# Kernel optimization log

Hardware: AMD Instinct MI355X
Metric: run time of the kernel (lower is better)

The kernel has to match this reference:

```python
import jax, jax.numpy as jnp
import numpy as np

FEATURE_DIM, HIDDEN_DIM, ATTN_DIM = 2048, 1024, 1024
B, L = 128, 196


def setup_inputs() -> dict:
    key = jax.random.key(0)
    ks = jax.random.split(key, 8)
    s_enc = 1.0 / np.sqrt(FEATURE_DIM)
    s_hid = 1.0 / np.sqrt(HIDDEN_DIM)
    s_full = 1.0 / np.sqrt(ATTN_DIM)
    return {
        "encoder_out": jax.random.normal(ks[0], (B, L, FEATURE_DIM), jnp.float32),
        "hidden": jax.random.normal(ks[1], (B, HIDDEN_DIM), jnp.float32),
        "W_enc": jax.random.uniform(ks[2], (FEATURE_DIM, ATTN_DIM), jnp.float32, -s_enc, s_enc),
        "b_enc": jax.random.uniform(ks[3], (ATTN_DIM,), jnp.float32, -s_enc, s_enc),
        "W_hid": jax.random.uniform(ks[4], (HIDDEN_DIM, ATTN_DIM), jnp.float32, -s_hid, s_hid),
        "b_hid": jax.random.uniform(ks[5], (ATTN_DIM,), jnp.float32, -s_hid, s_hid),
        "W_full": jax.random.uniform(ks[6], (ATTN_DIM,), jnp.float32, -s_full, s_full),
        "b_full": jax.random.uniform(ks[7], (1,), jnp.float32, -s_full, s_full),
    }


def reference(encoder_out, hidden, W_enc, b_enc, W_hid, b_hid, W_full, b_full):
    # attn1: (B, L, A)
    attn1 = jnp.einsum("blf,fa->bla", encoder_out, W_enc) + b_enc
    # attn2: (B, 1, A)
    attn2 = (hidden @ W_hid + b_hid)[:, None, :]
    attn = jax.nn.relu(attn1 + attn2)
    # scalar score per location: (B, L)
    scores = jnp.einsum("bla,a->bl", attn, W_full) + b_full[0]
    alpha = jax.nn.softmax(scores, axis=1)
    # weighted sum over L: (B, F)
    context = jnp.einsum("blf,bl->bf", encoder_out, alpha)
    return context, alpha
```

## Files before the change

kernel.cpp:

```cpp
#include <hip/hip_runtime.h>
#include <hip/hip_bf16.h>

typedef unsigned short u16;
typedef short s16x8 __attribute__((ext_vector_type(8)));
typedef unsigned int u32x4 __attribute__((ext_vector_type(4)));
typedef float f32x4 __attribute__((ext_vector_type(4)));

#define F_DIM 2048
#define A_DIM 1024
#define H_DIM 1024
#define BATCH 128
#define LLEN  196
#define MROWS (BATCH * LLEN)

__device__ __forceinline__ u16 f2b(float x) {
  union { float f; unsigned int u; } c; c.f = x;
  unsigned int r = (c.u + 0x7fffu + ((c.u >> 16) & 1u)) >> 16;
  return (u16)r;
}

__device__ __forceinline__ unsigned int f2b_pk(float a, float b) {
  unsigned int r;
  asm volatile("v_cvt_pk_bf16_f32 %0, %1, %2" : "=v"(r) : "v"(a), "v"(b));
  return r;
}

__device__ __forceinline__ void gload_lds16(const void* g, void* l) {
  __builtin_amdgcn_global_load_lds((const __attribute__((address_space(1))) void*)g,
                                   (__attribute__((address_space(3))) void*)l, 16, 0, 0);
}

__global__ void wenc_cvt_kernel(const float* __restrict__ W, u16* __restrict__ WT) {
  __shared__ float tile[32][33];
  int kb = blockIdx.x * 32, ab = blockIdx.y * 32;
  int t = threadIdx.x;
  int r = t >> 3, c = (t & 7) * 4;
  float4 v = *(const float4*)&W[(size_t)(kb + r) * A_DIM + ab + c];
  tile[r][c] = v.x; tile[r][c + 1] = v.y; tile[r][c + 2] = v.z; tile[r][c + 3] = v.w;
  __syncthreads();
  ushort4 o;
  o.x = f2b(tile[c + 0][r]);
  o.y = f2b(tile[c + 1][r]);
  o.z = f2b(tile[c + 2][r]);
  o.w = f2b(tile[c + 3][r]);
  *(ushort4*)&WT[(size_t)(ab + r) * F_DIM + kb + c] = o;
}

__global__ void attn2_kernel(const float* __restrict__ hidden, const float* __restrict__ W_hid,
                             const float* __restrict__ b_hid, const float* __restrict__ b_enc,
                             float* __restrict__ attn2p) {
  __shared__ float hl[8][128];
  int t = threadIdx.x;
  int a  = blockIdx.x * 256 + t;
  int b0 = blockIdx.y * 8;
  int k0 = blockIdx.z * 128;
  {
    int j = t >> 5, kk = (t & 31) * 4;
    float4 v = *(const float4*)&hidden[(size_t)(b0 + j) * H_DIM + k0 + kk];
    hl[j][kk + 0] = v.x; hl[j][kk + 1] = v.y; hl[j][kk + 2] = v.z; hl[j][kk + 3] = v.w;
  }
  __syncthreads();
  float acc[8] = {0.f, 0.f, 0.f, 0.f, 0.f, 0.f, 0.f, 0.f};
  #pragma unroll 4
  for (int k = 0; k < 128; ++k) {
    float w = W_hid[(size_t)(k0 + k) * A_DIM + a];
    #pragma unroll
    for (int j = 0; j < 8; ++j) acc[j] = fmaf(hl[j][k], w, acc[j]);
  }
  if (blockIdx.z == 0) {
    float bias = b_hid[a] + b_enc[a];
    #pragma unroll
    for (int j = 0; j < 8; ++j) acc[j] += bias;
  }
  #pragma unroll
  for (int j = 0; j < 8; ++j) atomicAdd(&attn2p[(size_t)(b0 + j) * A_DIM + a], acc[j]);
}

__global__ void gemm_score(const float* __restrict__ enc, const u16* __restrict__ WT,
                           const float* __restrict__ attn2p, const float* __restrict__ W_full,
                           float* __restrict__ scores) {
  __shared__ __align__(16) float Asf[128 * 32];
  __shared__ __align__(16) u16 Bs[128 * 32];
  __shared__ float wf_lds[128];
  __shared__ float at2_lds[2][128];

  int i = blockIdx.x;
  int g  = i >> 6;
  int r  = i & 63;
  int y  = r >> 3;
  int gi = r & 7;
  int mt = g * 8 + gi;
  if (mt >= MROWS / 128) return;

  int n0 = y * 128;
  int m0 = mt * 128;
  int t = threadIdx.x;

  int b0 = m0 / LLEN;
  int bnd = (b0 + 1) * LLEN;
  int b1 = min(b0 + 1, BATCH - 1);

  if (t < 128) {
    wf_lds[t] = W_full[n0 + t];
    at2_lds[0][t] = attn2p[(size_t)b0 * A_DIM + n0 + t];
    at2_lds[1][t] = attn2p[(size_t)b1 * A_DIM + n0 + t];
  }

  int lane = t & 63, wave = t >> 6;
  int wr = wave >> 1, wc = wave & 1;
  int c16 = lane & 15, quad = lane >> 4;

  f32x4 acc[4][4];
  #pragma unroll
  for (int ii = 0; ii < 4; ++ii)
    #pragma unroll
    for (int j = 0; j < 4; ++j) acc[ii][j] = (f32x4){0.f, 0.f, 0.f, 0.f};

  const float* agp = enc + (size_t)(m0 + wave * 32 + (lane >> 3)) * F_DIM
                         + ((lane & 7) ^ ((lane >> 3) & 7)) * 4;
  float* al = Asf + wave * 1024;
  const u16* bgp = WT + (size_t)(n0 + (t >> 2)) * F_DIM + ((t & 3) ^ ((t >> 3) & 3)) * 8;
  u16* bl = Bs + wave * 512;

  int akey = c16 & 7;
  int bkey = (c16 >> 1) & 3;

  for (int kt = 0; kt < F_DIM; kt += 32) {
    gload_lds16(agp + kt, al);
    gload_lds16(agp + (size_t)8 * F_DIM + kt, al + 256);
    gload_lds16(agp + (size_t)16 * F_DIM + kt, al + 512);
    gload_lds16(agp + (size_t)24 * F_DIM + kt, al + 768);
    gload_lds16(bgp + kt, bl);
    gload_lds16(bgp + (size_t)64 * F_DIM + kt, bl + 2048);
    __syncthreads();
    s16x8 af[4], bf[4];
    #pragma unroll
    for (int ii = 0; ii < 4; ++ii) {
      int arow = (wr * 64 + ii * 16 + c16) * 32;
      float4 lo = *(const float4*)&Asf[arow + ((2 * quad) ^ akey) * 4];
      float4 hi = *(const float4*)&Asf[arow + ((2 * quad + 1) ^ akey) * 4];
      u32x4 w;
      w.x = f2b_pk(lo.x, lo.y);
      w.y = f2b_pk(lo.z, lo.w);
      w.z = f2b_pk(hi.x, hi.y);
      w.w = f2b_pk(hi.z, hi.w);
      af[ii] = __builtin_bit_cast(s16x8, w);
      bf[ii] = *(const s16x8*)&Bs[(wc * 64 + ii * 16 + c16) * 32 + (quad ^ bkey) * 8];
    }
    #pragma unroll
    for (int mi = 0; mi < 4; ++mi)
      #pragma unroll
      for (int ni = 0; ni < 4; ++ni)
        acc[mi][ni] = __builtin_amdgcn_mfma_f32_16x16x32_bf16(af[mi], bf[ni], acc[mi][ni], 0, 0, 0);
    __syncthreads();
  }

  float wf[4], a2a[4], a2b[4];
  #pragma unroll
  for (int ni = 0; ni < 4; ++ni) {
    int col = wc * 64 + ni * 16 + c16;
    wf[ni] = wf_lds[col];
    a2a[ni] = at2_lds[0][col];
    a2b[ni] = at2_lds[1][col];
  }
  #pragma unroll
  for (int mi = 0; mi < 4; ++mi) {
    #pragma unroll
    for (int rr = 0; rr < 4; ++rr) {
      int row_g = m0 + wr * 64 + mi * 16 + quad * 4 + rr;
      bool hi = row_g >= bnd;
      float p = 0.f;
      #pragma unroll
      for (int ni = 0; ni < 4; ++ni) {
        float v = acc[mi][ni][rr] + (hi ? a2b[ni] : a2a[ni]);
        v = fmaxf(v, 0.f);
        p = fmaf(v, wf[ni], p);
      }
      p += __shfl_xor(p, 1);
      p += __shfl_xor(p, 2);
      p += __shfl_xor(p, 4);
      p += __shfl_xor(p, 8);
      if (c16 == 0) atomicAdd(&scores[row_g], p);
    }
  }
}

__global__ void softmax_kernel(const float* __restrict__ scores, float* __restrict__ alpha) {
  __shared__ float red[8];
  int b = blockIdx.x, t = threadIdx.x;
  float s = (t < LLEN) ? scores[b * LLEN + t] : -3.0e38f;
  float m = s;
  #pragma unroll
  for (int o = 1; o <= 32; o <<= 1) m = fmaxf(m, __shfl_xor(m, o));
  if ((t & 63) == 0) red[t >> 6] = m;
  __syncthreads();
  m = fmaxf(fmaxf(red[0], red[1]), fmaxf(red[2], red[3]));
  float e = (t < LLEN) ? expf(s - m) : 0.f;
  float sum = e;
  #pragma unroll
  for (int o = 1; o <= 32; o <<= 1) sum += __shfl_xor(sum, o);
  __syncthreads();
  if ((t & 63) == 0) red[4 + (t >> 6)] = sum;
  __syncthreads();
  sum = red[4] + red[5] + red[6] + red[7];
  if (t < LLEN) alpha[b * LLEN + t] = e / sum;
}

__global__ void context_kernel(const float* __restrict__ enc, const float* __restrict__ alpha,
                               float* __restrict__ out) {
  __shared__ float al[49];
  int b = blockIdx.y, t = threadIdx.x;
  int l0 = blockIdx.z * 49;
  int f4 = blockIdx.x * 256 + t;
  if (t < 49) al[t] = alpha[b * LLEN + l0 + t];
  __syncthreads();
  const float4* e4 = (const float4*)enc + ((size_t)b * LLEN + l0) * (F_DIM / 4) + f4;
  float4 acc = {0.f, 0.f, 0.f, 0.f};
  #pragma unroll 7
  for (int l = 0; l < 49; ++l) {
    float4 v = e4[(size_t)l * (F_DIM / 4)];
    float a = al[l];
    acc.x = fmaf(v.x, a, acc.x);
    acc.y = fmaf(v.y, a, acc.y);
    acc.z = fmaf(v.z, a, acc.z);
    acc.w = fmaf(v.w, a, acc.w);
  }
  float* o = out + (size_t)b * F_DIM + f4 * 4;
  atomicAdd(o + 0, acc.x);
  atomicAdd(o + 1, acc.y);
  atomicAdd(o + 2, acc.z);
  atomicAdd(o + 3, acc.w);
}

extern "C" void kernel_launch(void* const* d_in, const int* in_sizes, int n_in,
                              void* d_out, int out_size, void* d_ws, size_t ws_size,
                              hipStream_t stream) {
  const float* enc    = (const float*)d_in[0];
  const float* hidden = (const float*)d_in[1];
  const float* W_enc  = (const float*)d_in[2];
  const float* b_enc  = (const float*)d_in[3];
  const float* W_hid  = (const float*)d_in[4];
  const float* b_hid  = (const float*)d_in[5];
  const float* W_full = (const float*)d_in[6];
  float* out = (float*)d_out;
  float* alpha_out = out + (size_t)BATCH * F_DIM;

  const size_t wt_bytes = (size_t)A_DIM * F_DIM * sizeof(u16);
  const size_t a2_bytes = (size_t)BATCH * A_DIM * sizeof(float);
  const size_t sc_bytes = (size_t)MROWS * sizeof(float);
  char* ws = (char*)d_ws;
  u16*   WT     = (u16*)ws;
  float* attn2p = (float*)(ws + wt_bytes);
  float* scores = (float*)(ws + wt_bytes + a2_bytes);

  hipMemsetAsync(attn2p, 0, a2_bytes, stream);
  hipMemsetAsync(scores, 0, sc_bytes, stream);
  hipMemsetAsync(out, 0, (size_t)BATCH * F_DIM * sizeof(float), stream);

  wenc_cvt_kernel<<<dim3(F_DIM / 32, A_DIM / 32), 256, 0, stream>>>(W_enc, WT);
  attn2_kernel<<<dim3(A_DIM / 256, BATCH / 8, H_DIM / 128), 256, 0, stream>>>(hidden, W_hid, b_hid, b_enc, attn2p);
  gemm_score<<<dim3(1600), 256, 0, stream>>>(enc, WT, attn2p, W_full, scores);
  softmax_kernel<<<dim3(BATCH), 256, 0, stream>>>(scores, alpha_out);
  context_kernel<<<dim3(2, BATCH, 4), 256, 0, stream>>>(enc, alpha_out, out);
}
```

Before: 499.4 us.

## Rewrite score GEMM with 256x256 tiles and 4-stage register/LDS pipeline

The fused score GEMM now uses 256x256 output tiles with 512-thread blocks, which cuts redundant reloads of the fp32 encoder tile and of the bf16 weights. Encoder data is prefetched into registers, converted to bf16 once, and stored to LDS, so the per-wave repeated fp32-to-bf16 conversion at fragment load goes away. A 4-deep LDS ring with loads issued two to four k-steps ahead overlaps memory traffic with MFMA work, and s_setprio raises priority during the MFMA burst. The epilogue handles tiles that span up to three batch rows. In exchange, register pressure goes up with 32 accumulators per thread plus prefetch registers, LDS use grows to 128KB per block, and the grid shrinks to 416 blocks, which may hurt occupancy and load balance.

```diff
diff --git a/kernel.cpp b/kernel.cpp
--- a/kernel.cpp
+++ b/kernel.cpp
@@ -3,7 +3,7 @@
 
 typedef unsigned short u16;
 typedef short s16x8 __attribute__((ext_vector_type(8)));
-typedef unsigned int u32x4 __attribute__((ext_vector_type(4)));
+typedef unsigned int u32x2 __attribute__((ext_vector_type(2)));
 typedef float f32x4 __attribute__((ext_vector_type(4)));
 
 #define F_DIM 2048
@@ -12,6 +12,7 @@
 #define BATCH 128
 #define LLEN  196
 #define MROWS (BATCH * LLEN)
+#define MTILES (MROWS / 256)
 
 __device__ __forceinline__ u16 f2b(float x) {
   union { float f; unsigned int u; } c; c.f = x;
@@ -76,103 +77,137 @@
   for (int j = 0; j < 8; ++j) atomicAdd(&attn2p[(size_t)(b0 + j) * A_DIM + a], acc[j]);
 }
 
-__global__ void gemm_score(const float* __restrict__ enc, const u16* __restrict__ WT,
-                           const float* __restrict__ attn2p, const float* __restrict__ W_full,
-                           float* __restrict__ scores) {
-  __shared__ __align__(16) float Asf[128 * 32];
-  __shared__ __align__(16) u16 Bs[128 * 32];
-  __shared__ float wf_lds[128];
-  __shared__ float at2_lds[2][128];
+__global__ __launch_bounds__(512, 2) void gemm_score(
+    const float* __restrict__ enc, const u16* __restrict__ WT,
+    const float* __restrict__ attn2p, const float* __restrict__ W_full,
+    float* __restrict__ scores) {
+  __shared__ __align__(16) u16 As[4 * 8192];
+  __shared__ __align__(16) u16 Bs[4 * 8192];
 
   int i = blockIdx.x;
-  int g  = i >> 6;
-  int r  = i & 63;
-  int y  = r >> 3;
-  int gi = r & 7;
+  int g = i >> 5, r = i & 31;
+  int y = r >> 3, gi = r & 7;
   int mt = g * 8 + gi;
-  if (mt >= MROWS / 128) return;
-
-  int n0 = y * 128;
-  int m0 = mt * 128;
+  if (mt >= MTILES) return;
+  int m0 = mt * 256, n0 = y * 256;
   int t = threadIdx.x;
-
-  int b0 = m0 / LLEN;
-  int bnd = (b0 + 1) * LLEN;
-  int b1 = min(b0 + 1, BATCH - 1);
-
-  if (t < 128) {
-    wf_lds[t] = W_full[n0 + t];
-    at2_lds[0][t] = attn2p[(size_t)b0 * A_DIM + n0 + t];
-    at2_lds[1][t] = attn2p[(size_t)b1 * A_DIM + n0 + t];
-  }
-
   int lane = t & 63, wave = t >> 6;
-  int wr = wave >> 1, wc = wave & 1;
+  int wr = wave >> 2, wc = wave & 3;
   int c16 = lane & 15, quad = lane >> 4;
 
-  f32x4 acc[4][4];
-  #pragma unroll
-  for (int ii = 0; ii < 4; ++ii)
+  const float* aP = enc + (size_t)(m0 + (t >> 3)) * F_DIM + (t & 7) * 4;
+  const int awoff = (t >> 3) * 32 + ((((t & 7) >> 1) ^ (((t >> 3) >> 1) & 3)) * 8)
+                  + ((t & 7) & 1) * 4;
+  const u16* bP = WT + (size_t)(n0 + (t >> 2)) * F_DIM + ((t & 3) ^ ((t >> 3) & 3)) * 8;
+  const int bw512 = wave * 512;
+
+  const int akey = (c16 >> 1) & 3;
+  const int aroff = (wr * 128 + c16) * 32 + (quad ^ akey) * 8;
+  const int broff = (wc * 64 + c16) * 32 + (quad ^ akey) * 8;
+
+  f32x4 acc[8][4];
+  #pragma unroll
+  for (int mi = 0; mi < 8; ++mi)
     #pragma unroll
-    for (int j = 0; j < 4; ++j) acc[ii][j] = (f32x4){0.f, 0.f, 0.f, 0.f};
-
-  const float* agp = enc + (size_t)(m0 + wave * 32 + (lane >> 3)) * F_DIM
-                         + ((lane & 7) ^ ((lane >> 3) & 7)) * 4;
-  float* al = Asf + wave * 1024;
-  const u16* bgp = WT + (size_t)(n0 + (t >> 2)) * F_DIM + ((t & 3) ^ ((t >> 3) & 3)) * 8;
-  u16* bl = Bs + wave * 512;
-
-  int akey = c16 & 7;
-  int bkey = (c16 >> 1) & 3;
-
-  for (int kt = 0; kt < F_DIM; kt += 32) {
-    gload_lds16(agp + kt, al);
-    gload_lds16(agp + (size_t)8 * F_DIM + kt, al + 256);
-    gload_lds16(agp + (size_t)16 * F_DIM + kt, al + 512);
-    gload_lds16(agp + (size_t)24 * F_DIM + kt, al + 768);
-    gload_lds16(bgp + kt, bl);
-    gload_lds16(bgp + (size_t)64 * F_DIM + kt, bl + 2048);
-    __syncthreads();
-    s16x8 af[4], bf[4];
-    #pragma unroll
-    for (int ii = 0; ii < 4; ++ii) {
-      int arow = (wr * 64 + ii * 16 + c16) * 32;
-      float4 lo = *(const float4*)&Asf[arow + ((2 * quad) ^ akey) * 4];
-      float4 hi = *(const float4*)&Asf[arow + ((2 * quad + 1) ^ akey) * 4];
-      u32x4 w;
-      w.x = f2b_pk(lo.x, lo.y);
-      w.y = f2b_pk(lo.z, lo.w);
-      w.z = f2b_pk(hi.x, hi.y);
-      w.w = f2b_pk(hi.z, hi.w);
-      af[ii] = __builtin_bit_cast(s16x8, w);
-      bf[ii] = *(const s16x8*)&Bs[(wc * 64 + ii * 16 + c16) * 32 + (quad ^ bkey) * 8];
-    }
-    #pragma unroll
-    for (int mi = 0; mi < 4; ++mi)
-      #pragma unroll
-      for (int ni = 0; ni < 4; ++ni)
-        acc[mi][ni] = __builtin_amdgcn_mfma_f32_16x16x32_bf16(af[mi], bf[ni], acc[mi][ni], 0, 0, 0);
-    __syncthreads();
-  }
-
-  float wf[4], a2a[4], a2b[4];
+    for (int ni = 0; ni < 4; ++ni) acc[mi][ni] = (f32x4){0.f, 0.f, 0.f, 0.f};
+
+  float4 R0[4], R1[4];
+
+  #pragma unroll
+  for (int ii = 0; ii < 4; ++ii) R0[ii] = *(const float4*)(aP + (size_t)ii * 64 * F_DIM);
+  #pragma unroll
+  for (int ii = 0; ii < 4; ++ii) R1[ii] = *(const float4*)(aP + (size_t)ii * 64 * F_DIM + 32);
+  gload_lds16(bP, &Bs[bw512]);
+  gload_lds16(bP + (size_t)128 * F_DIM, &Bs[4096 + bw512]);
+  gload_lds16(bP + 32, &Bs[8192 + bw512]);
+  gload_lds16(bP + (size_t)128 * F_DIM + 32, &Bs[8192 + 4096 + bw512]);
+  #pragma unroll
+  for (int ii = 0; ii < 4; ++ii) {
+    u32x2 w; w.x = f2b_pk(R0[ii].x, R0[ii].y); w.y = f2b_pk(R0[ii].z, R0[ii].w);
+    *(u32x2*)&As[awoff + ii * 2048] = w;
+  }
+  #pragma unroll
+  for (int ii = 0; ii < 4; ++ii) {
+    u32x2 w; w.x = f2b_pk(R1[ii].x, R1[ii].y); w.y = f2b_pk(R1[ii].z, R1[ii].w);
+    *(u32x2*)&As[8192 + awoff + ii * 2048] = w;
+  }
+  #pragma unroll
+  for (int ii = 0; ii < 4; ++ii) R0[ii] = *(const float4*)(aP + (size_t)ii * 64 * F_DIM + 64);
+  #pragma unroll
+  for (int ii = 0; ii < 4; ++ii) R1[ii] = *(const float4*)(aP + (size_t)ii * 64 * F_DIM + 96);
+  asm volatile("s_waitcnt vmcnt(0) lgkmcnt(0)" ::: "memory");
+  __builtin_amdgcn_s_barrier();
+
+#define TILE(J, RX) do {                                                        \
+    const int rb_ = (J) * 8192;                                                 \
+    const int wb_ = (((J) + 2) & 3) * 8192;                                     \
+    int p_ = kt + (J);                                                          \
+    int kts_ = min(p_ + 2, 63);                                                 \
+    int ktl_ = min(p_ + 4, 63);                                                 \
+    _Pragma("unroll")                                                           \
+    for (int ii = 0; ii < 4; ++ii) {                                            \
+      u32x2 w_; w_.x = f2b_pk(RX[ii].x, RX[ii].y);                              \
+      w_.y = f2b_pk(RX[ii].z, RX[ii].w);                                        \
+      *(u32x2*)&As[wb_ + awoff + ii * 2048] = w_;                               \
+    }                                                                           \
+    _Pragma("unroll")                                                           \
+    for (int ii = 0; ii < 4; ++ii)                                              \
+      RX[ii] = *(const float4*)(aP + (size_t)ii * 64 * F_DIM + ktl_ * 32);      \
+    gload_lds16(bP + (size_t)kts_ * 32, &Bs[wb_ + bw512]);                      \
+    gload_lds16(bP + (size_t)128 * F_DIM + (size_t)kts_ * 32,                   \
+                &Bs[wb_ + 4096 + bw512]);                                       \
+    {                                                                           \
+      s16x8 af_[8], bf_[4];                                                     \
+      _Pragma("unroll")                                                         \
+      for (int ni = 0; ni < 4; ++ni)                                            \
+        bf_[ni] = *(const s16x8*)&Bs[rb_ + broff + ni * 512];                   \
+      _Pragma("unroll")                                                         \
+      for (int mi = 0; mi < 8; ++mi)                                            \
+        af_[mi] = *(const s16x8*)&As[rb_ + aroff + mi * 512];                   \
+      __builtin_amdgcn_s_setprio(1);                                            \
+      _Pragma("unroll")                                                         \
+      for (int mi = 0; mi < 8; ++mi)                                            \
+        _Pragma("unroll")                                                       \
+        for (int ni = 0; ni < 4; ++ni)                                          \
+          acc[mi][ni] = __builtin_amdgcn_mfma_f32_16x16x32_bf16(                \
+              af_[mi], bf_[ni], acc[mi][ni], 0, 0, 0);                          \
+      __builtin_amdgcn_s_setprio(0);                                            \
+    }                                                                           \
+    asm volatile("s_waitcnt vmcnt(6) lgkmcnt(0)" ::: "memory");                 \
+    __builtin_amdgcn_s_barrier();                                               \
+  } while (0)
+
+  #pragma unroll 1
+  for (int kt = 0; kt < 64; kt += 4) {
+    TILE(0, R0);
+    TILE(1, R1);
+    TILE(2, R0);
+    TILE(3, R1);
+  }
+#undef TILE
+
+  int bfirst = m0 / LLEN;
+  int bnd1 = (bfirst + 1) * LLEN, bnd2 = (bfirst + 2) * LLEN;
+  int b1c = min(bfirst + 1, BATCH - 1), b2c = min(bfirst + 2, BATCH - 1);
+  float wf[4], a2v0[4], a2v1[4], a2v2[4];
   #pragma unroll
   for (int ni = 0; ni < 4; ++ni) {
-    int col = wc * 64 + ni * 16 + c16;
-    wf[ni] = wf_lds[col];
-    a2a[ni] = at2_lds[0][col];
-    a2b[ni] = at2_lds[1][col];
-  }
-  #pragma unroll
-  for (int mi = 0; mi < 4; ++mi) {
+    int col = n0 + wc * 64 + ni * 16 + c16;
+    wf[ni]   = W_full[col];
+    a2v0[ni] = attn2p[(size_t)bfirst * A_DIM + col];
+    a2v1[ni] = attn2p[(size_t)b1c * A_DIM + col];
+    a2v2[ni] = attn2p[(size_t)b2c * A_DIM + col];
+  }
+  #pragma unroll
+  for (int mi = 0; mi < 8; ++mi) {
     #pragma unroll
     for (int rr = 0; rr < 4; ++rr) {
-      int row_g = m0 + wr * 64 + mi * 16 + quad * 4 + rr;
-      bool hi = row_g >= bnd;
+      int row_g = m0 + wr * 128 + mi * 16 + quad * 4 + rr;
       float p = 0.f;
       #pragma unroll
       for (int ni = 0; ni < 4; ++ni) {
-        float v = acc[mi][ni][rr] + (hi ? a2b[ni] : a2a[ni]);
+        float a2 = row_g >= bnd1 ? (row_g >= bnd2 ? a2v2[ni] : a2v1[ni]) : a2v0[ni];
+        float v = acc[mi][ni][rr] + a2;
         v = fmaxf(v, 0.f);
         p = fmaf(v, wf[ni], p);
       }
@@ -259,7 +294,7 @@
 
   wenc_cvt_kernel<<<dim3(F_DIM / 32, A_DIM / 32), 256, 0, stream>>>(W_enc, WT);
   attn2_kernel<<<dim3(A_DIM / 256, BATCH / 8, H_DIM / 128), 256, 0, stream>>>(hidden, W_hid, b_hid, b_enc, attn2p);
-  gemm_score<<<dim3(1600), 256, 0, stream>>>(enc, WT, attn2p, W_full, scores);
+  gemm_score<<<dim3(416), 512, 0, stream>>>(enc, WT, attn2p, W_full, scores);
   softmax_kernel<<<dim3(BATCH), 256, 0, stream>>>(scores, alpha_out);
   context_kernel<<<dim3(2, BATCH, 4), 256, 0, stream>>>(enc, alpha_out, out);
 }
```

After: 493.0 us. Within noise of the previous version (-1.3%).
